# Performance work log

Hardware: AMD Instinct MI355X
Metric: run time of the kernel (lower is better)

Reference implementation:

```python
import jax, jax.numpy as jnp
import numpy as np

V, E, HD, B, T, K = 50000, 256, 512, 64, 512, 16
H = HD // 2            # per-direction LSTM hidden size
START_IDX, STOP_IDX = K - 2, K - 1
NEG = -10000.0


def setup_inputs() -> dict:
    key = jax.random.key(0)
    ks = jax.random.split(key, 12)
    s = 0.05
    sentence = jax.random.randint(ks[0], (B, T), 0, V)
    emb = jax.random.normal(ks[1], (V, E), jnp.float32)
    w_ih_f = jax.random.normal(ks[2], (4 * H, E), jnp.float32) * s
    w_hh_f = jax.random.normal(ks[3], (4 * H, H), jnp.float32) * s
    b_f = jax.random.normal(ks[4], (4 * H,), jnp.float32) * s
    w_ih_b = jax.random.normal(ks[5], (4 * H, E), jnp.float32) * s
    w_hh_b = jax.random.normal(ks[6], (4 * H, H), jnp.float32) * s
    b_b = jax.random.normal(ks[7], (4 * H,), jnp.float32) * s
    w_out = jax.random.normal(ks[8], (K, HD), jnp.float32) * s
    b_out = jax.random.normal(ks[9], (K,), jnp.float32) * s
    transitions = jax.random.normal(ks[10], (K, K), jnp.float32)
    transitions = transitions.at[START_IDX, :].set(NEG)  # nothing transitions into START
    transitions = transitions.at[:, STOP_IDX].set(NEG)   # nothing transitions out of STOP
    return dict(sentence=sentence, emb=emb, w_ih_f=w_ih_f, w_hh_f=w_hh_f, b_f=b_f,
                w_ih_b=w_ih_b, w_hh_b=w_hh_b, b_b=b_b, w_out=w_out, b_out=b_out,
                transitions=transitions)


def _lstm(xs, w_ih, w_hh, b):
    # xs: [T, B, E] -> hs: [T, B, H]; PyTorch gate order i,f,g,o; bias b = b_ih + b_hh
    Bn = xs.shape[1]
    def step(carry, x):
        h, c = carry
        g = x @ w_ih.T + h @ w_hh.T + b
        i, f, gg, o = jnp.split(g, 4, axis=-1)
        c = jax.nn.sigmoid(f) * c + jax.nn.sigmoid(i) * jnp.tanh(gg)
        h = jax.nn.sigmoid(o) * jnp.tanh(c)
        return (h, c), h
    init = (jnp.zeros((Bn, H), xs.dtype), jnp.zeros((Bn, H), xs.dtype))
    return jax.lax.scan(step, init, xs)[1]


def _lstm_feats(sentence, emb, w_ih_f, w_hh_f, b_f, w_ih_b, w_hh_b, b_b, w_out, b_out):
    x = emb[sentence].transpose(1, 0, 2)                 # [T, B, E]
    hf = _lstm(x, w_ih_f, w_hh_f, b_f)                   # forward direction
    hb = _lstm(x[::-1], w_ih_b, w_hh_b, b_b)[::-1]       # backward direction
    h = jnp.concatenate([hf, hb], axis=-1)               # [T, B, HD]
    return h @ w_out.T + b_out                           # [T, B, K]


def _viterbi(feats, transitions):
    # feats: [T, B, K]
    Bn = feats.shape[1]
    init = jnp.full((Bn, K), NEG, jnp.float32).at[:, START_IDX].set(0.0)
    def vstep(fv, feat):
        scores = fv[:, None, :] + transitions[None, :, :]  # [B, next, prev]
        return jnp.max(scores, axis=2) + feat, jnp.argmax(scores, axis=2)
    fv, bptrs = jax.lax.scan(vstep, init, feats)           # bptrs: [T, B, K]
    terminal = fv + transitions[STOP_IDX][None, :]
    best_score = jnp.max(terminal, axis=1)                 # [B]
    best_tag = jnp.argmax(terminal, axis=1)                # [B]
    def bstep(tag, bptr):
        prev = jnp.take_along_axis(bptr, tag[:, None], axis=1)[:, 0]
        return prev, tag
    _, path = jax.lax.scan(bstep, best_tag, bptrs, reverse=True)  # [T, B]
    return best_score, path


def reference(sentence, emb, w_ih_f, w_hh_f, b_f, w_ih_b, w_hh_b, b_b, w_out, b_out, transitions):
    feats = _lstm_feats(sentence, emb, w_ih_f, w_hh_f, b_f, w_ih_b, w_hh_b, b_b, w_out, b_out)
    score, tag_seq = _viterbi(feats, transitions)
    return score, tag_seq
```

## Files before the change

kernel.cpp:

```cpp
#include <hip/hip_runtime.h>
#include <math.h>

typedef _Float16 h2_t  __attribute__((ext_vector_type(2)));
typedef _Float16 h8_t  __attribute__((ext_vector_type(8)));
typedef float    f4_t  __attribute__((ext_vector_type(4)));

#define T_ 512
#define B_ 64
#define E_ 256
#define H_ 256
#define G_ 1024
#define K_ 16
#define NEG_ (-10000.0f)
#define START_ 14
#define STOP_ 15

#if defined(__has_builtin)
#if __has_builtin(__builtin_amdgcn_fdot2)
#define HAVE_FDOT2 1
#endif
#endif

static __device__ __forceinline__ float dot2(h2_t a, h2_t b, float c) {
#ifdef HAVE_FDOT2
    return __builtin_amdgcn_fdot2(a, b, c, false);
#else
    return fmaf((float)a[0], (float)b[0], fmaf((float)a[1], (float)b[1], c));
#endif
}

template <int P, typename V>
static __device__ __forceinline__ h2_t get2(V v) {
    return __builtin_shufflevector(v, v, 2 * P, 2 * P + 1);
}

__global__ __launch_bounds__(256)
void prep_weights(const float* __restrict__ w_hh_f,
                  const float* __restrict__ w_hh_b,
                  const float* __restrict__ w_ih_f,
                  const float* __restrict__ w_ih_b,
                  _Float16* __restrict__ wreg2,
                  _Float16* __restrict__ wih16)
{
    const int blk = blockIdx.x, tid = threadIdx.x;
    if (blk < 64) {
        int e = blk * 256 + tid;
        int q = e & 511;
        int g = e >> 9;
        int d2 = g >> 3, v = g & 7;
        int dir = d2 >> 1, half = d2 & 1;
        int row = (q >> 7) * 256 + half * 128 + (q & 127);
        const float* src = (dir ? w_hh_b : w_hh_f) + (size_t)row * 256 + v * 32;
        _Float16* dst = wreg2 + (size_t)e * 32;
        #pragma unroll
        for (int i = 0; i < 32; ++i) dst[i] = (_Float16)src[i];
    } else {
        int idx = (blk - 64) * 256 + tid;
        int dir = idx / 32768, rem = idx % 32768;
        const float* src = (dir ? w_ih_b : w_ih_f) + (size_t)rem * 8;
        _Float16* dst = wih16 + (size_t)idx * 8;
        #pragma unroll
        for (int i = 0; i < 8; ++i) dst[i] = (_Float16)src[i];
    }
}

__global__ __launch_bounds__(256)
void gates_mfma(const int* __restrict__ sentence,
                const float* __restrict__ emb,
                const _Float16* __restrict__ wih16,
                _Float16* __restrict__ gin_f,
                _Float16* __restrict__ gin_b)
{
    __shared__ _Float16 As[64 * 264];
    __shared__ _Float16 Bs[256 * 40];
    __shared__ int sidx[64];

    const int bm  = blockIdx.x;
    const int dir = blockIdx.y;
    const int tid = threadIdx.x;

    const _Float16* __restrict__ wih = wih16 + (size_t)dir * 262144;
    _Float16* __restrict__ gout      = dir ? gin_b : gin_f;

    if (tid < 64) sidx[tid] = sentence[tid * T_ + bm];
    __syncthreads();

    {
        const int r = tid & 63, kq = tid >> 6;
        const float4* src = (const float4*)(emb + (size_t)sidx[r] * 256 + kq * 64);
        _Float16* dst = As + r * 264 + kq * 64;
        #pragma unroll
        for (int c = 0; c < 8; ++c) {
            float4 v0 = src[2 * c], v1 = src[2 * c + 1];
            h8_t o;
            o[0] = (_Float16)v0.x; o[1] = (_Float16)v0.y;
            o[2] = (_Float16)v0.z; o[3] = (_Float16)v0.w;
            o[4] = (_Float16)v1.x; o[5] = (_Float16)v1.y;
            o[6] = (_Float16)v1.z; o[7] = (_Float16)v1.w;
            *(h8_t*)(dst + c * 8) = o;
        }
    }

    const int wave = tid >> 6, lane = tid & 63;
    const int l15 = lane & 15, quad = lane >> 4;

    for (int pass = 0; pass < 4; ++pass) {
        const int n0 = pass * 256;
        f4_t acc[16];
        #pragma unroll
        for (int nt = 0; nt < 16; ++nt) acc[nt] = (f4_t){0.f, 0.f, 0.f, 0.f};

        for (int kc = 0; kc < 8; ++kc) {
            __syncthreads();
            {
                const h8_t* bsrc = (const h8_t*)(wih + (size_t)(n0 + tid) * 256 + kc * 32);
                #pragma unroll
                for (int c = 0; c < 4; ++c)
                    *(h8_t*)(Bs + tid * 40 + c * 8) = bsrc[c];
            }
            __syncthreads();
            h8_t a = *(const h8_t*)(As + (wave * 16 + l15) * 264 + kc * 32 + quad * 8);
            #pragma unroll
            for (int nt = 0; nt < 16; ++nt) {
                h8_t b = *(const h8_t*)(Bs + (nt * 16 + l15) * 40 + quad * 8);
                acc[nt] = __builtin_amdgcn_mfma_f32_16x16x32_f16(a, b, acc[nt], 0, 0, 0);
            }
        }

        const size_t mbase = (size_t)bm * 64 + wave * 16 + quad * 4;
        #pragma unroll
        for (int nt = 0; nt < 16; ++nt) {
            const int col = n0 + nt * 16 + l15;
            #pragma unroll
            for (int r = 0; r < 4; ++r)
                gout[(mbase + r) * 1024 + col] = (_Float16)acc[nt][r];
        }
    }
}

#define DOT8H(WC, HV, ACC) do {                                     \
    ACC = dot2(get2<0>(WC), get2<0>(HV), ACC);                      \
    ACC = dot2(get2<1>(WC), get2<1>(HV), ACC);                      \
    ACC = dot2(get2<2>(WC), get2<2>(HV), ACC);                      \
    ACC = dot2(get2<3>(WC), get2<3>(HV), ACC);                      \
} while (0)

#define VBLK(V, VI) do {                                            \
    h8_t hv0 = HB[(VI)*4+0], hv1 = HB[(VI)*4+1];                    \
    h8_t hv2 = HB[(VI)*4+2], hv3 = HB[(VI)*4+3];                    \
    DOT8H(W##V##_0, hv0, a0); DOT8H(W##V##_1, hv1, a1);             \
    DOT8H(W##V##_2, hv2, a2); DOT8H(W##V##_3, hv3, a3);             \
} while (0)

#define LDW(V)                                                      \
    h8_t W##V##_0 = b8[((V) * 512 + q) * 4 + 0],                    \
         W##V##_1 = b8[((V) * 512 + q) * 4 + 1],                    \
         W##V##_2 = b8[((V) * 512 + q) * 4 + 2],                    \
         W##V##_3 = b8[((V) * 512 + q) * 4 + 3]

__global__ __attribute__((amdgpu_flat_work_group_size(512, 512),
                          amdgpu_waves_per_eu(2, 2)))
void lstm_pair(const _Float16* __restrict__ gin_f,
               const _Float16* __restrict__ gin_b,
               const _Float16* __restrict__ wreg2,
               const float* __restrict__ b_f,
               const float* __restrict__ b_b,
               float* __restrict__ hf, float* __restrict__ hb,
               unsigned int* __restrict__ hex)
{
    __shared__ h8_t  hbuf8[32];
    __shared__ float gbuf[512];

    const int bid  = blockIdx.x;
    const int c16  = bid >> 4;
    const int w16  = bid & 15;
    const int half = w16 >> 3;
    const int pair = c16 * 8 + (w16 & 7);
    const int dir  = pair >> 6;
    const int b    = pair & 63;
    const int q    = threadIdx.x;

    const int gcl = q >> 7, off = q & 127;
    const int row = gcl * 256 + half * 128 + off;

    const _Float16* __restrict__ gin  = dir ? gin_b : gin_f;
    const float*    __restrict__ bs   = dir ? b_b : b_f;
    float*          __restrict__ hout = dir ? hb : hf;

    const h8_t* b8 = (const h8_t*)wreg2 + (size_t)(dir * 2 + half) * 16384;
    LDW(0); LDW(1); LDW(2); LDW(3); LDW(4); LDW(5); LDW(6); LDW(7);

    const float bias = bs[row];

    if (q < 32) hbuf8[q] = (h8_t)(_Float16)0.f;
    float c = 0.f;
    __syncthreads();

    const long tstr = 64 * 1024;
    const long hstr = 64 * 256;
    const int  t0   = dir ? (T_ - 1) : 0;
    const _Float16* gp = gin + (size_t)t0 * tstr + (size_t)b * 1024 + row;
    float*          hp = hout + (size_t)t0 * hstr + (size_t)b * 256 + half * 128 + q;
    const long gstep = dir ? -tstr : tstr;
    const long hstep = dir ? -hstr : hstr;

    unsigned int* hexPub = hex + (size_t)pair * 65536 + (size_t)half * 64 + (q >> 1);
    const int pi = (q >= 128 && q < 192) ? (q - 128) : 0;
    const unsigned int* hexPoll =
        hex + (size_t)pair * 65536 + (size_t)(1 - half) * 64 + pi;
    const int pdst = (1 - half) * 64 + pi;

    const h8_t* HB = hbuf8;
    unsigned int* hbufU = (unsigned int*)hbuf8;
    _Float16*    hbufH = (_Float16*)hbuf8;

    _Float16 gc0 = gp[0];

    for (int s = 0; s < T_; ++s) {
        _Float16 gn0 = gp[gstep];

        float a0 = 0.f, a1 = 0.f, a2 = 0.f, a3 = 0.f;
        VBLK(0, 0); VBLK(1, 1); VBLK(2, 2); VBLK(3, 3);
        VBLK(4, 4); VBLK(5, 5); VBLK(6, 6); VBLK(7, 7);

        gbuf[q] = bias + (float)gc0 + ((a0 + a1) + (a2 + a3));
        __syncthreads();

        if (q < 128) {
            float gi = gbuf[q], gf = gbuf[128 + q];
            float gg = gbuf[256 + q], go = gbuf[384 + q];
            float si = 1.f / (1.f + expf(-gi));
            float sf = 1.f / (1.f + expf(-gf));
            float so = 1.f / (1.f + expf(-go));
            c = sf * c + si * tanhf(gg);
            float h = so * tanhf(c);
            hp[0] = h;
            hbufH[half * 128 + q] = (_Float16)h;
            if (s < T_ - 1) {
                float hn = __shfl_down(h, 1, 64);
                if ((q & 1) == 0) {
                    h2_t pk; pk[0] = (_Float16)h; pk[1] = (_Float16)hn;
                    __hip_atomic_store(hexPub + (size_t)s * 128,
                                       __builtin_bit_cast(unsigned int, pk),
                                       __ATOMIC_RELAXED, __HIP_MEMORY_SCOPE_AGENT);
                }
            }
        } else if (q < 192 && s < T_ - 1) {
            const unsigned int* src = hexPoll + (size_t)s * 128;
            unsigned int u;
            int guard = 0;
            do {
                u = __hip_atomic_load(src, __ATOMIC_RELAXED,
                                      __HIP_MEMORY_SCOPE_AGENT);
            } while (u == 0xFFFFFFFFu && ++guard < (1 << 20));
            hbufU[pdst] = u;
        }
        gc0 = gn0;
        gp += gstep;
        hp += hstep;
        __syncthreads();
    }
}

__global__ __launch_bounds__(256)
void feats_proj(const float* __restrict__ hf, const float* __restrict__ hb,
                const float* __restrict__ w_out, const float* __restrict__ b_out,
                float* __restrict__ feats)
{
    const int lane = threadIdx.x & 63;
    const int wv   = threadIdx.x >> 6;
    const int m    = blockIdx.x * 4 + wv;
    const int o    = lane & 15;
    const int qq   = lane >> 4;

    const float* hsrc = (qq < 2) ? (hf + (size_t)m * 256 + qq * 128)
                                 : (hb + (size_t)m * 256 + (qq - 2) * 128);
    const float4* h4 = (const float4*)hsrc;
    const float4* w4 = (const float4*)(w_out + o * 512 + qq * 128);

    float acc = 0.f;
    #pragma unroll
    for (int i = 0; i < 32; ++i) {
        float4 hv = h4[i], wvv = w4[i];
        acc = fmaf(hv.x, wvv.x, acc);
        acc = fmaf(hv.y, wvv.y, acc);
        acc = fmaf(hv.z, wvv.z, acc);
        acc = fmaf(hv.w, wvv.w, acc);
    }
    acc += __shfl_xor(acc, 16, 64);
    acc += __shfl_xor(acc, 32, 64);
    if (lane < 16) feats[(size_t)m * 16 + o] = acc + b_out[o];
}

__global__ __launch_bounds__(64)
void viterbi(const float* __restrict__ feats, const float* __restrict__ trans,
             float* __restrict__ out)
{
    __shared__ unsigned char bp[T_][16];
    const int b    = blockIdx.x;
    const int lane = threadIdx.x;
    const int l15  = lane & 15;

    float tr[16];
    #pragma unroll
    for (int p = 0; p < 16; ++p)
        tr[p] = (lane < 16) ? trans[lane * 16 + p] : 0.f;

    float fv = (lane == START_) ? 0.f : NEG_;

    for (int t4 = 0; t4 < T_; t4 += 4) {
        float fblk = feats[((size_t)(t4 + (lane >> 4)) * 64 + b) * 16 + l15];
        #pragma unroll
        for (int tt = 0; tt < 4; ++tt) {
            const int t = t4 + tt;
            float best = -3.4e38f; int arg = 0;
            #pragma unroll
            for (int p = 0; p < 16; ++p) {
                float s = __shfl(fv, p, 64) + tr[p];
                if (s > best) { best = s; arg = p; }
            }
            float ft = __shfl(fblk, tt * 16 + l15, 64);
            if (lane < 16) {
                fv = best + ft;
                bp[t][lane] = (unsigned char)arg;
            }
        }
    }

    float term = fv + ((lane < 16) ? trans[STOP_ * 16 + lane] : 0.f);
    float v  = (lane < 16) ? term : -3.4e38f;
    int  idx = (lane < 16) ? lane : (1 << 20);
    #pragma unroll
    for (int off = 1; off < 64; off <<= 1) {
        float v2 = __shfl_xor(v, off, 64);
        int   i2 = __shfl_xor(idx, off, 64);
        if (v2 > v || (v2 == v && i2 < idx)) { v = v2; idx = i2; }
    }
    __syncthreads();
    if (lane == 0) {
        out[b] = v;
        int tag = idx;
        for (int t = T_ - 1; t >= 0; --t) {
            out[64 + (size_t)t * 64 + b] = (float)tag;
            tag = bp[t][tag];
        }
    }
}

extern "C" void kernel_launch(void* const* d_in, const int* in_sizes, int n_in,
                              void* d_out, int out_size, void* d_ws, size_t ws_size,
                              hipStream_t stream) {
    const int*   sentence = (const int*)d_in[0];
    const float* emb      = (const float*)d_in[1];
    const float* w_ih_f   = (const float*)d_in[2];
    const float* w_hh_f   = (const float*)d_in[3];
    const float* b_f      = (const float*)d_in[4];
    const float* w_ih_b   = (const float*)d_in[5];
    const float* w_hh_b   = (const float*)d_in[6];
    const float* b_b      = (const float*)d_in[7];
    const float* w_out    = (const float*)d_in[8];
    const float* b_out    = (const float*)d_in[9];
    const float* trans    = (const float*)d_in[10];
    float* out = (float*)d_out;

    _Float16* gin_f = (_Float16*)d_ws;
    _Float16* gin_b = gin_f + (size_t)T_ * B_ * G_;
    float* hf    = (float*)(gin_b + (size_t)T_ * B_ * G_);
    float* hb    = hf + (size_t)T_ * B_ * H_;
    float* feats = hb + (size_t)T_ * B_ * H_;
    _Float16* wih16 = (_Float16*)(feats + (size_t)T_ * B_ * K_);
    _Float16* wreg2 = wih16 + 524288;
    unsigned int* hex = (unsigned int*)(wreg2 + 524288);

    prep_weights<<<320, 256, 0, stream>>>(w_hh_f, w_hh_b, w_ih_f, w_ih_b,
                                          wreg2, wih16);
    gates_mfma<<<dim3(512, 2), 256, 0, stream>>>(sentence, emb, wih16,
                                                 gin_f, gin_b);
    hipMemsetAsync(hex, 0xFF, (size_t)33554432, stream);
    lstm_pair<<<256, 512, 0, stream>>>(gin_f, gin_b, wreg2, b_f, b_b,
                                       hf, hb, hex);
    feats_proj<<<8192, 256, 0, stream>>>(hf, hb, w_out, b_out, feats);
    viterbi<<<64, 64, 0, stream>>>(feats, trans, out);
}
```

Before: 1.357 ms.

## Split LSTM recurrent dot products over K halves with 1024-thread blocks

Doubles the lstm_pair block to 1024 threads. Each gate row's 256-long recurrent dot product is now split into two K-halves, each holding half the weights in registers, and the partial sums are combined through a doubled shared gate buffer before the activations. This halves the serial dot-product work per thread on every timestep of the critical recurrent path. In exchange it adds an extra shared-memory read per gate and runs more waves per block, which raises register and occupancy pressure.

```diff
diff --git a/kernel.cpp b/kernel.cpp
--- a/kernel.cpp
+++ b/kernel.cpp
@@ -145,21 +145,21 @@
     ACC = dot2(get2<3>(WC), get2<3>(HV), ACC);                      \
 } while (0)
 
-#define VBLK(V, VI) do {                                            \
-    h8_t hv0 = HB[(VI)*4+0], hv1 = HB[(VI)*4+1];                    \
-    h8_t hv2 = HB[(VI)*4+2], hv3 = HB[(VI)*4+3];                    \
+#define VBLK(V) do {                                                \
+    h8_t hv0 = HBk[(V)*4+0], hv1 = HBk[(V)*4+1];                    \
+    h8_t hv2 = HBk[(V)*4+2], hv3 = HBk[(V)*4+3];                    \
     DOT8H(W##V##_0, hv0, a0); DOT8H(W##V##_1, hv1, a1);             \
     DOT8H(W##V##_2, hv2, a2); DOT8H(W##V##_3, hv3, a3);             \
 } while (0)
 
 #define LDW(V)                                                      \
-    h8_t W##V##_0 = b8[((V) * 512 + q) * 4 + 0],                    \
-         W##V##_1 = b8[((V) * 512 + q) * 4 + 1],                    \
-         W##V##_2 = b8[((V) * 512 + q) * 4 + 2],                    \
-         W##V##_3 = b8[((V) * 512 + q) * 4 + 3]
-
-__global__ __attribute__((amdgpu_flat_work_group_size(512, 512),
-                          amdgpu_waves_per_eu(2, 2)))
+    h8_t W##V##_0 = b8k[((V) * 512 + qr) * 4 + 0],                  \
+         W##V##_1 = b8k[((V) * 512 + qr) * 4 + 1],                  \
+         W##V##_2 = b8k[((V) * 512 + qr) * 4 + 2],                  \
+         W##V##_3 = b8k[((V) * 512 + qr) * 4 + 3]
+
+__global__ __attribute__((amdgpu_flat_work_group_size(1024, 1024),
+                          amdgpu_waves_per_eu(4, 4)))
 void lstm_pair(const _Float16* __restrict__ gin_f,
                const _Float16* __restrict__ gin_b,
                const _Float16* __restrict__ wreg2,
@@ -169,7 +169,7 @@
                unsigned int* __restrict__ hex)
 {
     __shared__ h8_t  hbuf8[32];
-    __shared__ float gbuf[512];
+    __shared__ float gbuf[1024];
 
     const int bid  = blockIdx.x;
     const int c16  = bid >> 4;
@@ -179,16 +179,19 @@
     const int dir  = pair >> 6;
     const int b    = pair & 63;
     const int q    = threadIdx.x;
-
-    const int gcl = q >> 7, off = q & 127;
+    const int khalf = q >> 9;
+    const int qr    = q & 511;
+
+    const int gcl = qr >> 7, off = qr & 127;
     const int row = gcl * 256 + half * 128 + off;
 
     const _Float16* __restrict__ gin  = dir ? gin_b : gin_f;
     const float*    __restrict__ bs   = dir ? b_b : b_f;
     float*          __restrict__ hout = dir ? hb : hf;
 
-    const h8_t* b8 = (const h8_t*)wreg2 + (size_t)(dir * 2 + half) * 16384;
-    LDW(0); LDW(1); LDW(2); LDW(3); LDW(4); LDW(5); LDW(6); LDW(7);
+    const h8_t* b8k = (const h8_t*)wreg2 + (size_t)(dir * 2 + half) * 16384
+                                          + (size_t)khalf * 8192;
+    LDW(0); LDW(1); LDW(2); LDW(3);
 
     const float bias = bs[row];
 
@@ -205,30 +208,36 @@
     const long hstep = dir ? -hstr : hstr;
 
     unsigned int* hexPub = hex + (size_t)pair * 65536 + (size_t)half * 64 + (q >> 1);
-    const int pi = (q >= 128 && q < 192) ? (q - 128) : 0;
+    const int pollw = (q >= 128 && q < 192);
+    const int pi = pollw ? (q - 128) : 0;
     const unsigned int* hexPoll =
         hex + (size_t)pair * 65536 + (size_t)(1 - half) * 64 + pi;
     const int pdst = (1 - half) * 64 + pi;
 
-    const h8_t* HB = hbuf8;
+    const h8_t* HBk = hbuf8 + khalf * 16;
     unsigned int* hbufU = (unsigned int*)hbuf8;
     _Float16*    hbufH = (_Float16*)hbuf8;
 
-    _Float16 gc0 = gp[0];
+    _Float16 gc0 = (_Float16)0.f;
+    if (!khalf) gc0 = gp[0];
 
     for (int s = 0; s < T_; ++s) {
-        _Float16 gn0 = gp[gstep];
+        _Float16 gn0 = (_Float16)0.f;
+        if (!khalf) gn0 = gp[gstep];
 
         float a0 = 0.f, a1 = 0.f, a2 = 0.f, a3 = 0.f;
-        VBLK(0, 0); VBLK(1, 1); VBLK(2, 2); VBLK(3, 3);
-        VBLK(4, 4); VBLK(5, 5); VBLK(6, 6); VBLK(7, 7);
-
-        gbuf[q] = bias + (float)gc0 + ((a0 + a1) + (a2 + a3));
+        VBLK(0); VBLK(1); VBLK(2); VBLK(3);
+
+        float part = (a0 + a1) + (a2 + a3);
+        if (!khalf) part += bias + (float)gc0;
+        gbuf[q] = part;
         __syncthreads();
 
         if (q < 128) {
-            float gi = gbuf[q], gf = gbuf[128 + q];
-            float gg = gbuf[256 + q], go = gbuf[384 + q];
+            float gi = gbuf[q]       + gbuf[q + 512];
+            float gf = gbuf[q + 128] + gbuf[q + 640];
+            float gg = gbuf[q + 256] + gbuf[q + 768];
+            float go = gbuf[q + 384] + gbuf[q + 896];
             float si = 1.f / (1.f + expf(-gi));
             float sf = 1.f / (1.f + expf(-gf));
             float so = 1.f / (1.f + expf(-go));
@@ -245,7 +254,7 @@
                                        __ATOMIC_RELAXED, __HIP_MEMORY_SCOPE_AGENT);
                 }
             }
-        } else if (q < 192 && s < T_ - 1) {
+        } else if (pollw && s < T_ - 1) {
             const unsigned int* src = hexPoll + (size_t)s * 128;
             unsigned int u;
             int guard = 0;
@@ -377,8 +386,8 @@
     gates_mfma<<<dim3(512, 2), 256, 0, stream>>>(sentence, emb, wih16,
                                                  gin_f, gin_b);
     hipMemsetAsync(hex, 0xFF, (size_t)33554432, stream);
-    lstm_pair<<<256, 512, 0, stream>>>(gin_f, gin_b, wreg2, b_f, b_b,
-                                       hf, hb, hex);
+    lstm_pair<<<256, 1024, 0, stream>>>(gin_f, gin_b, wreg2, b_f, b_b,
+                                        hf, hb, hex);
     feats_proj<<<8192, 256, 0, stream>>>(hf, hb, w_out, b_out, feats);
     viterbi<<<64, 64, 0, stream>>>(feats, trans, out);
 }
```

Result: no change. 1.370 ms (+0.9%).
